# Kernel optimization log

Hardware: AMD Instinct MI355X
Metric: run time of the kernel (lower is better)

Reference implementation:

```python
import jax, jax.numpy as jnp
import numpy as np

D_MODEL = 1024
N_HEADS = 16
D_K = 64
D_FF = 4 * D_MODEL
LN_EPS = 1e-5


def _ln(x, g, b):
    mu = jnp.mean(x, axis=-1, keepdims=True)
    var = jnp.mean((x - mu) ** 2, axis=-1, keepdims=True)
    return (x - mu) * jax.lax.rsqrt(var + LN_EPS) * g + b


def setup_inputs() -> dict:
    key = jax.random.key(0)
    ks = jax.random.split(key, 24)
    d, h, dk, dff = D_MODEL, N_HEADS, D_K, D_FF
    s = lambda k, sh, fan: jax.random.normal(k, sh, jnp.float32) / np.sqrt(fan)
    return {
        "x": jax.random.normal(ks[0], (2, 2048, d), jnp.float32),
        "mask": jnp.ones((2, 2048), jnp.int32),
        # pre-attention q/k/v embed linears (d -> d)
        "Wqe": s(ks[1], (d, d), d), "bqe": jnp.zeros((d,), jnp.float32),
        "Wke": s(ks[2], (d, d), d), "bke": jnp.zeros((d,), jnp.float32),
        "Wve": s(ks[3], (d, d), d), "bve": jnp.zeros((d,), jnp.float32),
        # MHA projections (d -> h*dk) and output fc
        "Wq": s(ks[4], (d, h * dk), d), "bq": jnp.zeros((h * dk,), jnp.float32),
        "Wk": s(ks[5], (d, h * dk), d), "bk": jnp.zeros((h * dk,), jnp.float32),
        "Wv": s(ks[6], (d, h * dk), d), "bv": jnp.zeros((h * dk,), jnp.float32),
        "Wo": s(ks[7], (h * dk, d), h * dk), "bo": jnp.zeros((d,), jnp.float32),
        # layer norms
        "g1": jnp.ones((d,), jnp.float32), "b1": jnp.zeros((d,), jnp.float32),
        "g2": jnp.ones((d,), jnp.float32), "b2": jnp.zeros((d,), jnp.float32),
        # FFN
        "W1": s(ks[8], (d, dff), d), "bb1": jnp.zeros((dff,), jnp.float32),
        "W2": s(ks[9], (dff, d), dff), "bb2": jnp.zeros((d,), jnp.float32),
    }


def reference(x, mask, Wqe, bqe, Wke, bke, Wve, bve, Wq, bq, Wk, bk, Wv, bv,
              Wo, bo, g1, b1, g2, b2, W1, bb1, W2, bb2):
    N, T, _ = x.shape
    h, dk = N_HEADS, D_K
    # pre-embeds then MHA projections
    q = ((x @ Wqe + bqe) @ Wq + bq).reshape(N, T, h, dk)
    k = ((x @ Wke + bke) @ Wk + bk).reshape(N, T, h, dk)
    v = ((x @ Wve + bve) @ Wv + bv).reshape(N, T, h, dk)
    scores = jnp.einsum("bthd,bshd->bhts", q, k) / np.sqrt(dk).astype(np.float32)
    scores = jnp.where(mask[:, None, None, :] == 0, -jnp.inf, scores)
    attn = jax.nn.softmax(scores, axis=-1)
    a = jnp.einsum("bhts,bshd->bthd", attn, v).reshape(N, T, h * dk)
    mha_out = a @ Wo + bo
    x = _ln(x + mha_out, g1, b1)
    ffn = jax.nn.gelu(x @ W1 + bb1, approximate=False) @ W2 + bb2
    x = _ln(x + ffn, g2, b2)
    return x  # dropout is identity in eval mode
```

## Files before the change

kernel.cpp:

```cpp
#include <hip/hip_runtime.h>
#include <stdint.h>
#include <math.h>


#define DM   1024
#define DFF  4096
#define NH   16
#define DKH  64
#define TSEQ 2048
#define TOK  4096

using f32x4  = float  __attribute__((ext_vector_type(4)));
using bf16x8 = __bf16 __attribute__((ext_vector_type(8)));
using s16x8  = short  __attribute__((ext_vector_type(8)));

typedef const void __attribute__((address_space(1)))* gas_ptr;
typedef void       __attribute__((address_space(3)))* las_ptr;

__device__ __forceinline__ short f2bf(float f) {
  unsigned u; __builtin_memcpy(&u, &f, 4);
  u += 0x7FFFu + ((u >> 16) & 1u);
  return (short)(u >> 16);
}
__device__ __forceinline__ float bf2f(short s) {
  unsigned u = ((unsigned)(unsigned short)s) << 16;
  float f; __builtin_memcpy(&f, &u, 4);
  return f;
}
__device__ __forceinline__ unsigned cvt_pk_bf16(float lo, float hi) {
  unsigned r;
  asm volatile("v_cvt_pk_bf16_f32 %0, %1, %2" : "=v"(r) : "v"(lo), "v"(hi));
  return r;
}
__device__ __forceinline__ f32x4 mfma16(s16x8 a, s16x8 b, f32x4 c) {
  return __builtin_amdgcn_mfma_f32_16x16x32_bf16(
      __builtin_bit_cast(bf16x8, a), __builtin_bit_cast(bf16x8, b), c, 0, 0, 0);
}
__device__ __forceinline__ void gload16(const void* g, void* l) {
  __builtin_amdgcn_global_load_lds((gas_ptr)g, (las_ptr)l, 16, 0, 0);
}
__device__ __forceinline__ float gelu_f(float x) {
  float u = x * (0.7978845608f + 0.0356774081f * x * x);
  float e = exp2f(u * 2.8853900818f);
  return x - x / (1.f + e);
}

struct CvtArgs { const float* S[4]; short* D[4]; long n[4]; };
__global__ void cvt_bf16_b(CvtArgs a) {
  const int z = blockIdx.y;
  long i = ((long)blockIdx.x * 256 + threadIdx.x) * 8;
  if (i >= a.n[z]) return;
  const float* S = a.S[z]; short* D = a.D[z];
  float4 va = *(const float4*)(S + i);
  float4 vb = *(const float4*)(S + i + 4);
  s16x8 o;
  o[0]=f2bf(va.x); o[1]=f2bf(va.y); o[2]=f2bf(va.z); o[3]=f2bf(va.w);
  o[4]=f2bf(vb.x); o[5]=f2bf(vb.y); o[6]=f2bf(vb.z); o[7]=f2bf(vb.w);
  *(s16x8*)(D + i) = o;
}

struct TcvtArgs { const float* W[4]; short* WT[4]; };
template<int NZ>
__global__ __launch_bounds__(256) void transpose_cvt(TcvtArgs a, int R, int C) {
  __shared__ float t[64][65];
  const int z = (NZ > 1) ? blockIdx.z : 0;
  const float* __restrict__ W = a.W[z];
  short* __restrict__ WT = a.WT[z];
  const int c0 = blockIdx.x * 64, r0 = blockIdx.y * 64;
  const int tr = threadIdx.x >> 4, tc = (threadIdx.x & 15) * 4;
  #pragma unroll
  for (int q = 0; q < 4; q++) {
    int rr = q * 16 + tr;
    float4 v = *(const float4*)(W + (long)(r0 + rr) * C + c0 + tc);
    t[rr][tc] = v.x; t[rr][tc+1] = v.y; t[rr][tc+2] = v.z; t[rr][tc+3] = v.w;
  }
  __syncthreads();
  #pragma unroll
  for (int q = 0; q < 4; q++) {
    int rr = q * 16 + tr;
    short4 o;
    o.x = f2bf(t[tc+0][rr]); o.y = f2bf(t[tc+1][rr]);
    o.z = f2bf(t[tc+2][rr]); o.w = f2bf(t[tc+3][rr]);
    *(short4*)(WT + (long)(c0 + rr) * R + r0 + tc) = o;
  }
}

struct BiasArgs {
  const float* be[3]; const short* WT[3]; const float* b2[3]; float* bc[3]; int K;
};
__global__ void fuse_bias(BiasArgs a) {
  const int z = blockIdx.y, n = blockIdx.x, lane = threadIdx.x;
  const float* be = a.be[z];
  const short* WT = a.WT[z] + (long)n * a.K;
  float s = 0.f;
  for (int k = lane; k < a.K; k += 64) s += be[k] * bf2f(WT[k]);
  #pragma unroll
  for (int d = 1; d < 64; d <<= 1) s += __shfl_xor(s, d);
  if (lane == 0) a.bc[z][n] = s + a.b2[z][n];
}

struct GemmArgs {
  const short* A[3]; const short* B[3]; const float* bias[3]; void* C[6];
  float oscale[3];
  int M, N, K;
  int tmask;
  int zshift;
};

template<int EPI>
__global__ __launch_bounds__(256) void gemm_bt(GemmArgs g) {
  const int zz = blockIdx.z;
  const int prob = zz >> g.zshift;
  const int slice = zz & ((1 << g.zshift) - 1);
  const short* __restrict__ A = g.A[prob];
  const short* __restrict__ B = g.B[prob];
  const float* __restrict__ bias = g.bias[prob];
  const int N = g.N, K = g.K;
  const int Ks = K >> g.zshift;
  const int kbase = slice * Ks;
  const int tn = blockIdx.x * 128, tm = blockIdx.y * 128;
  const int tid = threadIdx.x;
  const int lane = tid & 63, w = tid >> 6;
  const int wr = w >> 1, wc = w & 1;
  const int g2 = lane >> 4, q = lane & 15;

  __shared__ alignas(16) short lbuf[4][128 * 64];

  f32x4 acc[4][4] = {};

  const int srow = lane >> 3;
  const int scol = lane & 7;

  auto STAGE = [&](int k0, int bf) {
    #pragma unroll
    for (int qq = 0; qq < 4; qq++) {
      const int row  = w * 32 + qq * 8 + srow;
      const int slot = scol ^ (row & 7);
      gload16(A + (long)(tm + row) * K + kbase + k0 + slot * 8,
              &lbuf[bf][(w * 32 + qq * 8) * 64]);
      gload16(B + (long)(tn + row) * K + kbase + k0 + slot * 8,
              &lbuf[2 + bf][(w * 32 + qq * 8) * 64]);
    }
  };

  STAGE(0, 0);
  __syncthreads();

  const int nk = Ks >> 6;
  #pragma unroll 2
  for (int it = 0; it < nk; it++) {
    const int cur = it & 1;
    if (it + 1 < nk) STAGE((it + 1) << 6, cur ^ 1);

    const short* cA = &lbuf[cur][0];
    const short* cB = &lbuf[2 + cur][0];
    #pragma unroll
    for (int kk = 0; kk < 2; kk++) {
      s16x8 af[4], bfr[4];
      #pragma unroll
      for (int m = 0; m < 4; m++) {
        const int row = wr * 64 + m * 16 + q;
        const int ps  = (kk * 4 + g2) ^ (row & 7);
        af[m] = *(const s16x8*)(cA + row * 64 + ps * 8);
      }
      #pragma unroll
      for (int n = 0; n < 4; n++) {
        const int row = wc * 64 + n * 16 + q;
        const int ps  = (kk * 4 + g2) ^ (row & 7);
        bfr[n] = *(const s16x8*)(cB + row * 64 + ps * 8);
      }
      __builtin_amdgcn_s_setprio(1);
      #pragma unroll
      for (int m = 0; m < 4; m++)
        #pragma unroll
        for (int n = 0; n < 4; n++)
          acc[m][n] = mfma16(af[m], bfr[n], acc[m][n]);
      __builtin_amdgcn_s_setprio(0);
    }
    __syncthreads();
  }

  const bool outT = (g.tmask >> prob) & 1;
  const float sc = g.oscale[prob];
  float bv[4];
  #pragma unroll
  for (int n = 0; n < 4; n++)
    bv[n] = bias ? bias[tn + wc * 64 + n * 16 + q] : 0.f;

  if (EPI == 1) {
    float* C = (float*)g.C[zz];
    #pragma unroll
    for (int n = 0; n < 4; n++) {
      const int col = tn + wc * 64 + n * 16 + q;
      #pragma unroll
      for (int m = 0; m < 4; m++) {
        const int row0 = tm + wr * 64 + m * 16 + g2 * 4;
        #pragma unroll
        for (int r = 0; r < 4; r++)
          C[(long)(row0 + r) * N + col] = (acc[m][n][r] + bv[n]) * sc;
      }
    }
  } else {
    short* lC = &lbuf[0][0];
    short* C = (short*)g.C[zz];
    #pragma unroll
    for (int h2 = 0; h2 < 2; h2++) {
      __syncthreads();
      if (!outT ? (wr == h2) : (wc == h2)) {
        #pragma unroll
        for (int m = 0; m < 4; m++)
          #pragma unroll
          for (int n = 0; n < 4; n++)
            #pragma unroll
            for (int r = 0; r < 4; r++) {
              float xv = (acc[m][n][r] + bv[n]) * sc;
              if (EPI == 2) xv = gelu_f(xv);
              if (!outT) {
                const int rl = m * 16 + g2 * 4 + r;
                const int cl = wc * 64 + n * 16 + q;
                lC[rl * 136 + cl] = f2bf(xv);
              } else {
                const int cl = n * 16 + q;
                const int rl = wr * 64 + m * 16 + g2 * 4 + r;
                lC[cl * 136 + rl] = f2bf(xv);
              }
            }
      }
      __syncthreads();
      const int lrow = tid >> 4, l16 = tid & 15;
      #pragma unroll
      for (int rr = 0; rr < 4; rr++) {
        const int row = rr * 16 + lrow;
        s16x8 vv = *(const s16x8*)(lC + row * 136 + l16 * 8);
        if (!outT)
          *(s16x8*)(C + (long)(tm + h2 * 64 + row) * N + tn + l16 * 8) = vv;
        else
          *(s16x8*)(C + (long)(tn + h2 * 64 + row) * g.M + tm + l16 * 8) = vv;
      }
    }
  }
}

struct Gemm256Args {
  const short* A[3]; const short* B[3]; const float* bias[3]; void* C[3];
  float oscale[3];
  int M, N, K;
  int tmask;
};

template<int EPI>
__global__ __launch_bounds__(512, 2) void gemm256(Gemm256Args g) {
  const int prob = blockIdx.z;
  const short* __restrict__ A = g.A[prob];
  const short* __restrict__ B = g.B[prob];
  const float* __restrict__ bias = g.bias[prob];
  const int N = g.N, K = g.K;

  const int gx = gridDim.x;
  const int nwg = gx * gridDim.y;
  const int bid = blockIdx.y * gx + blockIdx.x;
  const int cpx = nwg >> 3;
  const int tile = (bid & 7) * cpx + (bid >> 3);
  const int tn = (tile % gx) * 256, tm = (tile / gx) * 256;

  const int tid = threadIdx.x;
  const int lane = tid & 63, w = tid >> 6;
  const int wr = w >> 2, wc = w & 3;
  const int g2 = lane >> 4, q = lane & 15;
  const int srow = lane >> 3, scol = lane & 7;

  __shared__ alignas(16) short lA[2][256 * 64];
  __shared__ alignas(16) short lB[2][256 * 64];

  f32x4 acc[8][4] = {};

  auto STAGE = [&](int kb, int bf) {
    #pragma unroll
    for (int qq = 0; qq < 4; qq++) {
      const int row  = w * 32 + qq * 8 + srow;
      const int slot = scol ^ (row & 7);
      gload16(A + (long)(tm + row) * K + kb + slot * 8, &lA[bf][(w * 32 + qq * 8) * 64]);
      gload16(B + (long)(tn + row) * K + kb + slot * 8, &lB[bf][(w * 32 + qq * 8) * 64]);
    }
  };

  STAGE(0, 0);
  __syncthreads();

  const int nk = K >> 6;
  #pragma unroll 2
  for (int it = 0; it < nk; it++) {
    const int cur = it & 1;
    if (it + 1 < nk) STAGE((it + 1) << 6, cur ^ 1);

    const short* cA = &lA[cur][0];
    const short* cB = &lB[cur][0];
    s16x8 bfr[4][2];
    #pragma unroll
    for (int n = 0; n < 4; n++)
      #pragma unroll
      for (int kk = 0; kk < 2; kk++) {
        const int row = wc * 64 + n * 16 + q;
        const int ps  = (kk * 4 + g2) ^ (row & 7);
        bfr[n][kk] = *(const s16x8*)(cB + row * 64 + ps * 8);
      }
    __builtin_amdgcn_s_setprio(1);
    #pragma unroll
    for (int m = 0; m < 8; m++) {
      s16x8 af[2];
      #pragma unroll
      for (int kk = 0; kk < 2; kk++) {
        const int row = wr * 128 + m * 16 + q;
        const int ps  = (kk * 4 + g2) ^ (row & 7);
        af[kk] = *(const s16x8*)(cA + row * 64 + ps * 8);
      }
      #pragma unroll
      for (int kk = 0; kk < 2; kk++)
        #pragma unroll
        for (int n = 0; n < 4; n++)
          acc[m][n] = mfma16(af[kk], bfr[n][kk], acc[m][n]);
    }
    __builtin_amdgcn_s_setprio(0);
    __syncthreads();
  }

  short* lC = &lA[0][0];
  short* C = (short*)g.C[prob];
  const bool outT = (g.tmask >> prob) & 1;
  const float sc = g.oscale[prob];
  float bv[4];
  #pragma unroll
  for (int n = 0; n < 4; n++)
    bv[n] = bias ? bias[tn + wc * 64 + n * 16 + q] : 0.f;

  #pragma unroll
  for (int p = 0; p < 4; p++) {
    __syncthreads();
    if (!outT) {
      if (wr == (p >> 1)) {
        const int mb = (p & 1) * 4;
        #pragma unroll
        for (int mm = 0; mm < 4; mm++)
          #pragma unroll
          for (int n = 0; n < 4; n++)
            #pragma unroll
            for (int r = 0; r < 4; r++) {
              float xv = (acc[mb + mm][n][r] + bv[n]) * sc;
              if (EPI == 2) xv = gelu_f(xv);
              lC[(mm * 16 + g2 * 4 + r) * 272 + wc * 64 + n * 16 + q] = f2bf(xv);
            }
      }
    } else {
      if (wc == p) {
        #pragma unroll
        for (int m = 0; m < 8; m++)
          #pragma unroll
          for (int n = 0; n < 4; n++)
            #pragma unroll
            for (int r = 0; r < 4; r++) {
              float xv = (acc[m][n][r] + bv[n]) * sc;
              lC[(n * 16 + q) * 272 + wr * 128 + m * 16 + g2 * 4 + r] = f2bf(xv);
            }
      }
    }
    __syncthreads();
    #pragma unroll
    for (int rr = 0; rr < 4; rr++) {
      const int row = rr * 16 + (tid >> 5);
      s16x8 vv = *(const s16x8*)(lC + row * 272 + (tid & 31) * 8);
      if (!outT)
        *(s16x8*)(C + (long)(tm + p * 64 + row) * N + tn + (tid & 31) * 8) = vv;
      else
        *(s16x8*)(C + (long)(tn + p * 64 + row) * g.M + tm + (tid & 31) * 8) = vv;
    }
  }
}

__global__ __launch_bounds__(512) void flash_attn(const short* __restrict__ Q,
                                                  const short* __restrict__ Km,
                                                  const short* __restrict__ VT,
                                                  const int* __restrict__ mask,
                                                  short* __restrict__ O) {
  const int qt = blockIdx.x;
  const int bh = blockIdx.y;
  const int b = bh >> 4, h = bh & 15;
  const int tid = threadIdx.x;
  const int lane = tid & 63, w = tid >> 6;
  const int g2 = lane >> 4, q = lane & 15;

  __shared__ alignas(16) short lK[2][64 * 64];
  __shared__ alignas(16) short lV[2][64 * 64];
  __shared__ alignas(16) short lP[8][16 * 64];

  const int qrow0 = b * TSEQ + qt * 128 + w * 16;

  s16x8 qf[2];
  #pragma unroll
  for (int kk = 0; kk < 2; kk++)
    qf[kk] = *(const s16x8*)(Q + (long)(qrow0 + q) * DM + h * DKH + kk * 32 + g2 * 8);

  f32x4 oacc[4] = {};
  f32x4 dacc = {};
  s16x8 vones;
  #pragma unroll
  for (int j = 0; j < 8; j++) vones[j] = (short)0x3F80;

  const int srow = lane >> 3, scol = lane & 7;
  const int strow = w * 8 + srow;
  const int sslot = scol ^ (strow & 7);
  short* lPw = &lP[w][0];
  const int psw = (q & 7) << 3;

  const int nt = TSEQ / 64;
  gload16(Km + (long)(b * TSEQ + strow) * DM + h * DKH + sslot * 8,
          &lK[0][(w * 8) * 64]);
  gload16(VT + (long)(h * DKH + strow) * TOK + b * TSEQ + sslot * 8,
          &lV[0][(w * 8) * 64]);

  #pragma unroll 2
  for (int t = 0; t < nt; t++) {
    const int cb = t & 1;
    const short* lKc = &lK[cb][0];
    const short* lVc = &lV[cb][0];
    __syncthreads();

    if (t + 1 < nt) {
      const int kvn = (t + 1) * 64;
      gload16(Km + (long)(b * TSEQ + kvn + strow) * DM + h * DKH + sslot * 8,
              &lK[cb ^ 1][(w * 8) * 64]);
      gload16(VT + (long)(h * DKH + strow) * TOK + b * TSEQ + kvn + sslot * 8,
              &lV[cb ^ 1][(w * 8) * 64]);
    }
    const int mk = mask[b * TSEQ + t * 64 + lane];

    f32x4 s[4] = {};
    __builtin_amdgcn_s_setprio(1);
    #pragma unroll
    for (int kk = 0; kk < 2; kk++)
      #pragma unroll
      for (int n = 0; n < 4; n++) {
        const int row = n * 16 + q;
        const int ps  = (kk * 4 + g2) ^ (row & 7);
        s16x8 kf = *(const s16x8*)(lKc + row * 64 + ps * 8);
        s[n] = mfma16(kf, qf[kk], s[n]);
      }
    __builtin_amdgcn_s_setprio(0);

    float p[4][4];
    #pragma unroll
    for (int n = 0; n < 4; n++)
      #pragma unroll
      for (int r = 0; r < 4; r++)
        p[n][r] = exp2f(s[n][r]);

    if (__ballot(mk == 0)) {
      const float mzf = mk ? 1.f : 0.f;
      #pragma unroll
      for (int n = 0; n < 4; n++)
        #pragma unroll
        for (int r = 0; r < 4; r++)
          p[n][r] *= __shfl(mzf, n * 16 + g2 * 4 + r);
    }

    #pragma unroll
    for (int n = 0; n < 4; n++)
      #pragma unroll
      for (int hh = 0; hh < 2; hh++) {
        unsigned pk = cvt_pk_bf16(p[n][2 * hh], p[n][2 * hh + 1]);
        *(unsigned*)(lPw + ((q * 64 + n * 16 + g2 * 4 + 2 * hh) ^ psw)) = pk;
      }
    s16x8 pf[2];
    #pragma unroll
    for (int kk = 0; kk < 2; kk++)
      pf[kk] = *(const s16x8*)(lPw + ((q * 64 + kk * 32 + g2 * 8) ^ psw));

    __builtin_amdgcn_s_setprio(1);
    #pragma unroll
    for (int kk = 0; kk < 2; kk++) {
      #pragma unroll
      for (int n = 0; n < 4; n++) {
        const int row = n * 16 + q;
        const int ps  = (kk * 4 + g2) ^ (row & 7);
        s16x8 vf = *(const s16x8*)(lVc + row * 64 + ps * 8);
        oacc[n] = mfma16(pf[kk], vf, oacc[n]);
      }
      dacc = mfma16(pf[kk], vones, dacc);
    }
    __builtin_amdgcn_s_setprio(0);
  }

  float rI[4];
  #pragma unroll
  for (int r = 0; r < 4; r++) rI[r] = 1.f / dacc[r];
  #pragma unroll
  for (int n = 0; n < 4; n++) {
    const int col = h * DKH + n * 16 + q;
    #pragma unroll
    for (int r = 0; r < 4; r++) {
      const int row = qrow0 + g2 * 4 + r;
      O[(long)row * DM + col] = f2bf(oacc[n][r] * rI[r]);
    }
  }
}

template<bool WB16>
__global__ __launch_bounds__(256) void ln_residual(const float* __restrict__ X,
                                                   const float* __restrict__ P0,
                                                   const float* __restrict__ P1,
                                                   const float* __restrict__ rbias,
                                                   const float* __restrict__ gw,
                                                   const float* __restrict__ bw,
                                                   float* __restrict__ Yf,
                                                   short* __restrict__ Yb) {
  const int row = blockIdx.x, tid = threadIdx.x;
  const float4 xv = *(const float4*)(X + (long)row * DM + tid * 4);
  const float4 p0 = *(const float4*)(P0 + (long)row * DM + tid * 4);
  const float4 p1 = *(const float4*)(P1 + (long)row * DM + tid * 4);
  const float4 rb = *(const float4*)(rbias + tid * 4);
  float v[4] = {xv.x + p0.x + p1.x + rb.x, xv.y + p0.y + p1.y + rb.y,
                xv.z + p0.z + p1.z + rb.z, xv.w + p0.w + p1.w + rb.w};
  float s  = v[0] + v[1] + v[2] + v[3];
  float s2 = v[0]*v[0] + v[1]*v[1] + v[2]*v[2] + v[3]*v[3];
  #pragma unroll
  for (int d = 1; d < 64; d <<= 1) { s += __shfl_xor(s, d); s2 += __shfl_xor(s2, d); }
  __shared__ float red[8];
  const int lane = tid & 63, w = tid >> 6;
  if (lane == 0) { red[w] = s; red[w + 4] = s2; }
  __syncthreads();
  s  = red[0] + red[1] + red[2] + red[3];
  s2 = red[4] + red[5] + red[6] + red[7];
  const float mu  = s * (1.f / DM);
  const float inv = rsqrtf(s2 * (1.f / DM) - mu * mu + 1e-5f);
  #pragma unroll
  for (int i = 0; i < 4; i++) {
    const int col = tid * 4 + i;
    const float y = (v[i] - mu) * inv * gw[col] + bw[col];
    Yf[(long)row * DM + col] = y;
    if (WB16) Yb[(long)row * DM + col] = f2bf(y);
  }
}

extern "C" void kernel_launch(void* const* d_in, const int* in_sizes, int n_in,
                              void* d_out, int out_size, void* d_ws, size_t ws_size,
                              hipStream_t stream) {
  const float* x   = (const float*)d_in[0];
  const int*   msk = (const int*)d_in[1];
  const float* Wqe = (const float*)d_in[2];  const float* bqe = (const float*)d_in[3];
  const float* Wke = (const float*)d_in[4];  const float* bke = (const float*)d_in[5];
  const float* Wve = (const float*)d_in[6];  const float* bve = (const float*)d_in[7];
  const float* Wq  = (const float*)d_in[8];  const float* bq  = (const float*)d_in[9];
  const float* Wk  = (const float*)d_in[10]; const float* bk  = (const float*)d_in[11];
  const float* Wv  = (const float*)d_in[12]; const float* bv  = (const float*)d_in[13];
  const float* Wo  = (const float*)d_in[14]; const float* bo  = (const float*)d_in[15];
  const float* g1  = (const float*)d_in[16]; const float* b1  = (const float*)d_in[17];
  const float* g2  = (const float*)d_in[18]; const float* b2  = (const float*)d_in[19];
  const float* W1  = (const float*)d_in[20]; const float* bb1 = (const float*)d_in[21];
  const float* W2  = (const float*)d_in[22]; const float* bb2 = (const float*)d_in[23];

  char* ws = (char*)d_ws;
  const size_t MB = 1024ull * 1024ull;
  short* xb   = (short*)(ws + 0);
  short* woT  = (short*)(ws + 8 * MB);
  short* w1T  = (short*)(ws + 10 * MB);
  short* w2T  = (short*)(ws + 18 * MB);
  short* wqeB = (short*)(ws + 26 * MB);
  short* wkeB = (short*)(ws + 28 * MB);
  short* wveB = (short*)(ws + 30 * MB);
  short* wqT  = (short*)(ws + 32 * MB);
  short* wkT  = (short*)(ws + 34 * MB);
  short* wvT  = (short*)(ws + 36 * MB);
  short* wcqT = (short*)(ws + 38 * MB);
  short* wckT = (short*)(ws + 40 * MB);
  short* wcvT = (short*)(ws + 42 * MB);
  float* bcq  = (float*)(ws + 44 * MB);
  float* bck  = (float*)(ws + 44 * MB + 16384);
  float* bcv  = (float*)(ws + 44 * MB + 32768);
  short* Qb   = (short*)(ws + 45 * MB);
  short* Kb2  = (short*)(ws + 53 * MB);
  short* VTb  = (short*)(ws + 61 * MB);
  float* mhaP0= (float*)(ws + 26 * MB);
  float* mhaP1= (float*)(ws + 42 * MB);
  short* Hb   = (short*)(ws + 26 * MB);
  float* yf   = (float*)(ws + 58 * MB);
  short* ybf  = (short*)(ws + 74 * MB);
  float* ffnP0= (float*)d_out;
  float* ffnP1= (float*)(ws + 0);
  short* Aout = xb;

  CvtArgs ca = {};
  ca.S[0] = x;  ca.D[0] = xb;   ca.n[0] = (long)TOK * DM;
  ca.S[1] = Wqe; ca.D[1] = wqeB; ca.n[1] = (long)DM * DM;
  ca.S[2] = Wke; ca.D[2] = wkeB; ca.n[2] = (long)DM * DM;
  ca.S[3] = Wve; ca.D[3] = wveB; ca.n[3] = (long)DM * DM;
  cvt_bf16_b<<<dim3((long)TOK * DM / 2048, 4), 256, 0, stream>>>(ca);

  TcvtArgs t4 = {};
  t4.W[0] = Wq; t4.WT[0] = wqT;  t4.W[1] = Wk; t4.WT[1] = wkT;
  t4.W[2] = Wv; t4.WT[2] = wvT;  t4.W[3] = Wo; t4.WT[3] = woT;
  transpose_cvt<4><<<dim3(16, 16, 4), 256, 0, stream>>>(t4, DM, DM);
  TcvtArgs t1 = {}; t1.W[0] = W1; t1.WT[0] = w1T;
  transpose_cvt<1><<<dim3(64, 16), 256, 0, stream>>>(t1, DM, DFF);
  TcvtArgs t2 = {}; t2.W[0] = W2; t2.WT[0] = w2T;
  transpose_cvt<1><<<dim3(16, 64), 256, 0, stream>>>(t2, DFF, DM);

  GemmArgs fa = {};
  fa.A[0] = wqT;  fa.A[1] = wkT;  fa.A[2] = wvT;
  fa.B[0] = wqeB; fa.B[1] = wkeB; fa.B[2] = wveB;
  fa.C[0] = wcqT; fa.C[1] = wckT; fa.C[2] = wcvT;
  fa.oscale[0] = 1.f; fa.oscale[1] = 1.f; fa.oscale[2] = 1.f;
  fa.M = DM; fa.N = DM; fa.K = DM; fa.tmask = 0; fa.zshift = 0;
  gemm_bt<0><<<dim3(8, 8, 3), 256, 0, stream>>>(fa);

  BiasArgs ba = {};
  ba.be[0] = bqe; ba.be[1] = bke; ba.be[2] = bve;
  ba.WT[0] = wqT; ba.WT[1] = wkT; ba.WT[2] = wvT;
  ba.b2[0] = bq;  ba.b2[1] = bk;  ba.b2[2] = bv;
  ba.bc[0] = bcq; ba.bc[1] = bck; ba.bc[2] = bcv; ba.K = DM;
  fuse_bias<<<dim3(DM, 3), 64, 0, stream>>>(ba);

  Gemm256Args qa = {};
  qa.A[0] = xb;   qa.A[1] = xb;   qa.A[2] = xb;
  qa.B[0] = wcqT; qa.B[1] = wckT; qa.B[2] = wcvT;
  qa.bias[0] = bcq; qa.bias[1] = bck; qa.bias[2] = bcv;
  qa.C[0] = Qb; qa.C[1] = Kb2; qa.C[2] = VTb;
  qa.oscale[0] = 0.125f * 1.44269504f; qa.oscale[1] = 1.f; qa.oscale[2] = 1.f;
  qa.M = TOK; qa.N = DM; qa.K = DM; qa.tmask = 4;
  gemm256<0><<<dim3(4, 16, 3), 512, 0, stream>>>(qa);

  flash_attn<<<dim3(TSEQ / 128, 2 * NH), 512, 0, stream>>>(Qb, Kb2, VTb, msk, Aout);

  GemmArgs oa = {};
  oa.A[0] = Aout; oa.B[0] = woT; oa.bias[0] = nullptr;
  oa.C[0] = mhaP0; oa.C[1] = mhaP1;
  oa.oscale[0] = 1.f;
  oa.M = TOK; oa.N = DM; oa.K = DM; oa.tmask = 0; oa.zshift = 1;
  gemm_bt<1><<<dim3(8, 32, 2), 256, 0, stream>>>(oa);

  ln_residual<true><<<dim3(TOK), 256, 0, stream>>>(x, mhaP0, mhaP1, bo,
                                                   g1, b1, yf, ybf);

  Gemm256Args f1 = {};
  f1.A[0] = ybf; f1.B[0] = w1T; f1.bias[0] = bb1; f1.C[0] = Hb;
  f1.oscale[0] = 1.f;
  f1.M = TOK; f1.N = DFF; f1.K = DM; f1.tmask = 0;
  gemm256<2><<<dim3(16, 16, 1), 512, 0, stream>>>(f1);

  GemmArgs f2 = {};
  f2.A[0] = Hb; f2.B[0] = w2T; f2.bias[0] = nullptr;
  f2.C[0] = ffnP0; f2.C[1] = ffnP1;
  f2.oscale[0] = 1.f;
  f2.M = TOK; f2.N = DM; f2.K = DFF; f2.tmask = 0; f2.zshift = 1;
  gemm_bt<1><<<dim3(8, 32, 2), 256, 0, stream>>>(f2);

  ln_residual<false><<<dim3(TOK), 256, 0, stream>>>(yf, ffnP0, ffnP1, bb2,
                                                    g2, b2, (float*)d_out, nullptr);
}
```

Baseline: 292.3 us.

## Use 128-wide KV tiles in flash attention and merge weight transpose launches

Flash attention now stages 128 keys/values per iteration instead of 64, which halves the number of loop iterations and barriers. The P·V step is split into two 64-column halves that reuse the per-wave P scratch, and launch_bounds now requests two blocks per CU. The three weight transpose-convert launches are merged into one 3072-block launch that decodes matrix and tile from the block index, saving launch overhead. The larger shared-memory tiles and wider score registers raise register and LDS pressure, which could limit occupancy.

```diff
diff --git a/kernel.cpp b/kernel.cpp
--- a/kernel.cpp
+++ b/kernel.cpp
@@ -59,14 +59,17 @@
   *(s16x8*)(D + i) = o;
 }
 
-struct TcvtArgs { const float* W[4]; short* WT[4]; };
-template<int NZ>
-__global__ __launch_bounds__(256) void transpose_cvt(TcvtArgs a, int R, int C) {
+struct Tcvt6Args { const float* W[6]; short* WT[6]; };
+__global__ __launch_bounds__(256) void transpose_cvt6(Tcvt6Args a) {
   __shared__ float t[64][65];
-  const int z = (NZ > 1) ? blockIdx.z : 0;
+  const int bid = blockIdx.x;
+  int z, bx, by, R, C;
+  if (bid < 1024)      { z = bid >> 8; int u = bid & 255;  bx = u & 15; by = u >> 4; R = 1024; C = 1024; }
+  else if (bid < 2048) { z = 4;        int u = bid - 1024; bx = u & 63; by = u >> 6; R = 1024; C = 4096; }
+  else                 { z = 5;        int u = bid - 2048; bx = u & 15; by = u >> 4; R = 4096; C = 1024; }
   const float* __restrict__ W = a.W[z];
   short* __restrict__ WT = a.WT[z];
-  const int c0 = blockIdx.x * 64, r0 = blockIdx.y * 64;
+  const int c0 = bx * 64, r0 = by * 64;
   const int tr = threadIdx.x >> 4, tc = (threadIdx.x & 15) * 4;
   #pragma unroll
   for (int q = 0; q < 4; q++) {
@@ -376,11 +379,11 @@
   }
 }
 
-__global__ __launch_bounds__(512) void flash_attn(const short* __restrict__ Q,
-                                                  const short* __restrict__ Km,
-                                                  const short* __restrict__ VT,
-                                                  const int* __restrict__ mask,
-                                                  short* __restrict__ O) {
+__global__ __launch_bounds__(512, 2) void flash_attn(const short* __restrict__ Q,
+                                                     const short* __restrict__ Km,
+                                                     const short* __restrict__ VT,
+                                                     const int* __restrict__ mask,
+                                                     short* __restrict__ O) {
   const int qt = blockIdx.x;
   const int bh = blockIdx.y;
   const int b = bh >> 4, h = bh & 15;
@@ -388,8 +391,8 @@
   const int lane = tid & 63, w = tid >> 6;
   const int g2 = lane >> 4, q = lane & 15;
 
-  __shared__ alignas(16) short lK[2][64 * 64];
-  __shared__ alignas(16) short lV[2][64 * 64];
+  __shared__ alignas(16) short lK[2][128 * 64];
+  __shared__ alignas(16) short lV[2][64 * 128];
   __shared__ alignas(16) short lP[8][16 * 64];
 
   const int qrow0 = b * TSEQ + qt * 128 + w * 16;
@@ -405,40 +408,47 @@
   #pragma unroll
   for (int j = 0; j < 8; j++) vones[j] = (short)0x3F80;
 
-  const int srow = lane >> 3, scol = lane & 7;
-  const int strow = w * 8 + srow;
-  const int sslot = scol ^ (strow & 7);
+  const int srow8 = lane >> 3, scol8 = lane & 7;
+  const int srow16 = lane >> 4, scol16 = lane & 15;
+  const int kr0 = w * 16 + srow8, kr1 = kr0 + 8;
+  const int ks0 = scol8 ^ (kr0 & 7), ks1 = scol8 ^ (kr1 & 7);
+  const int vr0 = w * 4 + srow16, vr1 = vr0 + 32;
+  const int vs0 = scol16 ^ (vr0 & 15), vs1 = scol16 ^ (vr1 & 15);
+
   short* lPw = &lP[w][0];
   const int psw = (q & 7) << 3;
 
-  const int nt = TSEQ / 64;
-  gload16(Km + (long)(b * TSEQ + strow) * DM + h * DKH + sslot * 8,
-          &lK[0][(w * 8) * 64]);
-  gload16(VT + (long)(h * DKH + strow) * TOK + b * TSEQ + sslot * 8,
-          &lV[0][(w * 8) * 64]);
-
-  #pragma unroll 2
+  auto STAGE = [&](int kvb, int bf) {
+    gload16(Km + (long)(b * TSEQ + kvb + kr0) * DM + h * DKH + ks0 * 8,
+            &lK[bf][(w * 16) * 64]);
+    gload16(Km + (long)(b * TSEQ + kvb + kr1) * DM + h * DKH + ks1 * 8,
+            &lK[bf][(w * 16 + 8) * 64]);
+    gload16(VT + (long)(h * DKH + vr0) * TOK + b * TSEQ + kvb + vs0 * 8,
+            &lV[bf][(w * 4) * 128]);
+    gload16(VT + (long)(h * DKH + vr1) * TOK + b * TSEQ + kvb + vs1 * 8,
+            &lV[bf][(32 + w * 4) * 128]);
+  };
+
+  STAGE(0, 0);
+
+  const int nt = TSEQ / 128;
   for (int t = 0; t < nt; t++) {
     const int cb = t & 1;
     const short* lKc = &lK[cb][0];
     const short* lVc = &lV[cb][0];
     __syncthreads();
 
-    if (t + 1 < nt) {
-      const int kvn = (t + 1) * 64;
-      gload16(Km + (long)(b * TSEQ + kvn + strow) * DM + h * DKH + sslot * 8,
-              &lK[cb ^ 1][(w * 8) * 64]);
-      gload16(VT + (long)(h * DKH + strow) * TOK + b * TSEQ + kvn + sslot * 8,
-              &lV[cb ^ 1][(w * 8) * 64]);
-    }
-    const int mk = mask[b * TSEQ + t * 64 + lane];
-
-    f32x4 s[4] = {};
+    if (t + 1 < nt) STAGE((t + 1) * 128, cb ^ 1);
+    const int mbase = b * TSEQ + t * 128;
+    const int mk0 = mask[mbase + lane];
+    const int mk1 = mask[mbase + 64 + lane];
+
+    f32x4 s[8] = {};
     __builtin_amdgcn_s_setprio(1);
     #pragma unroll
     for (int kk = 0; kk < 2; kk++)
       #pragma unroll
-      for (int n = 0; n < 4; n++) {
+      for (int n = 0; n < 8; n++) {
         const int row = n * 16 + q;
         const int ps  = (kk * 4 + g2) ^ (row & 7);
         s16x8 kf = *(const s16x8*)(lKc + row * 64 + ps * 8);
@@ -446,47 +456,52 @@
       }
     __builtin_amdgcn_s_setprio(0);
 
-    float p[4][4];
-    #pragma unroll
-    for (int n = 0; n < 4; n++)
+    #pragma unroll
+    for (int n = 0; n < 8; n++)
       #pragma unroll
       for (int r = 0; r < 4; r++)
-        p[n][r] = exp2f(s[n][r]);
-
-    if (__ballot(mk == 0)) {
-      const float mzf = mk ? 1.f : 0.f;
+        s[n][r] = exp2f(s[n][r]);
+
+    if (__ballot(mk0 == 0) | __ballot(mk1 == 0)) {
+      const float mz0 = mk0 ? 1.f : 0.f;
+      const float mz1 = mk1 ? 1.f : 0.f;
       #pragma unroll
       for (int n = 0; n < 4; n++)
         #pragma unroll
-        for (int r = 0; r < 4; r++)
-          p[n][r] *= __shfl(mzf, n * 16 + g2 * 4 + r);
-    }
-
-    #pragma unroll
-    for (int n = 0; n < 4; n++)
-      #pragma unroll
-      for (int hh = 0; hh < 2; hh++) {
-        unsigned pk = cvt_pk_bf16(p[n][2 * hh], p[n][2 * hh + 1]);
-        *(unsigned*)(lPw + ((q * 64 + n * 16 + g2 * 4 + 2 * hh) ^ psw)) = pk;
-      }
-    s16x8 pf[2];
-    #pragma unroll
-    for (int kk = 0; kk < 2; kk++)
-      pf[kk] = *(const s16x8*)(lPw + ((q * 64 + kk * 32 + g2 * 8) ^ psw));
-
-    __builtin_amdgcn_s_setprio(1);
-    #pragma unroll
-    for (int kk = 0; kk < 2; kk++) {
-      #pragma unroll
-      for (int n = 0; n < 4; n++) {
-        const int row = n * 16 + q;
-        const int ps  = (kk * 4 + g2) ^ (row & 7);
-        s16x8 vf = *(const s16x8*)(lVc + row * 64 + ps * 8);
-        oacc[n] = mfma16(pf[kk], vf, oacc[n]);
-      }
-      dacc = mfma16(pf[kk], vones, dacc);
-    }
-    __builtin_amdgcn_s_setprio(0);
+        for (int r = 0; r < 4; r++) {
+          s[n][r]     *= __shfl(mz0, n * 16 + g2 * 4 + r);
+          s[n + 4][r] *= __shfl(mz1, n * 16 + g2 * 4 + r);
+        }
+    }
+
+    #pragma unroll
+    for (int hf = 0; hf < 2; hf++) {
+      #pragma unroll
+      for (int n = 0; n < 4; n++)
+        #pragma unroll
+        for (int hh = 0; hh < 2; hh++) {
+          unsigned pk = cvt_pk_bf16(s[hf * 4 + n][2 * hh], s[hf * 4 + n][2 * hh + 1]);
+          *(unsigned*)(lPw + ((q * 64 + n * 16 + g2 * 4 + 2 * hh) ^ psw)) = pk;
+        }
+      s16x8 pf[2];
+      #pragma unroll
+      for (int kk = 0; kk < 2; kk++)
+        pf[kk] = *(const s16x8*)(lPw + ((q * 64 + kk * 32 + g2 * 8) ^ psw));
+
+      __builtin_amdgcn_s_setprio(1);
+      #pragma unroll
+      for (int kk = 0; kk < 2; kk++) {
+        #pragma unroll
+        for (int n = 0; n < 4; n++) {
+          const int row = n * 16 + q;
+          const int ps  = ((hf * 2 + kk) * 4 + g2) ^ (row & 15);
+          s16x8 vf = *(const s16x8*)(lVc + row * 128 + ps * 8);
+          oacc[n] = mfma16(pf[kk], vf, oacc[n]);
+        }
+        dacc = mfma16(pf[kk], vones, dacc);
+      }
+      __builtin_amdgcn_s_setprio(0);
+    }
   }
 
   float rI[4];
@@ -594,14 +609,11 @@
   ca.S[3] = Wve; ca.D[3] = wveB; ca.n[3] = (long)DM * DM;
   cvt_bf16_b<<<dim3((long)TOK * DM / 2048, 4), 256, 0, stream>>>(ca);
 
-  TcvtArgs t4 = {};
-  t4.W[0] = Wq; t4.WT[0] = wqT;  t4.W[1] = Wk; t4.WT[1] = wkT;
-  t4.W[2] = Wv; t4.WT[2] = wvT;  t4.W[3] = Wo; t4.WT[3] = woT;
-  transpose_cvt<4><<<dim3(16, 16, 4), 256, 0, stream>>>(t4, DM, DM);
-  TcvtArgs t1 = {}; t1.W[0] = W1; t1.WT[0] = w1T;
-  transpose_cvt<1><<<dim3(64, 16), 256, 0, stream>>>(t1, DM, DFF);
-  TcvtArgs t2 = {}; t2.W[0] = W2; t2.WT[0] = w2T;
-  transpose_cvt<1><<<dim3(16, 64), 256, 0, stream>>>(t2, DFF, DM);
+  Tcvt6Args t6 = {};
+  t6.W[0] = Wq; t6.WT[0] = wqT;  t6.W[1] = Wk; t6.WT[1] = wkT;
+  t6.W[2] = Wv; t6.WT[2] = wvT;  t6.W[3] = Wo; t6.WT[3] = woT;
+  t6.W[4] = W1; t6.WT[4] = w1T;  t6.W[5] = W2; t6.WT[5] = w2T;
+  transpose_cvt6<<<dim3(3072), 256, 0, stream>>>(t6);
 
   GemmArgs fa = {};
   fa.A[0] = wqT;  fa.A[1] = wkT;  fa.A[2] = wvT;
```

New measurement: 287.2 us. Within noise of the previous version (-1.8%).
